# Kernel optimization log

Measured on AMD Instinct MI355X. Metric: run time of the kernel, lower is better.

The kernel has to match this reference:

```python
import jax, jax.numpy as jnp
import numpy as np

B, S, H, F, E, K = 2, 2048, 1024, 4096, 8, 2
NH = H // 128  # heads of dim 128, per SimpleMoEBlock.__init__
DH = H // NH


def _layernorm(x, g, b, eps=1e-5):
    m = x.mean(-1, keepdims=True)
    v = ((x - m) ** 2).mean(-1, keepdims=True)
    return (x - m) / jnp.sqrt(v + eps) * g + b


def _forward(x, ln_attn_g, ln_attn_b, ln_mlp_g, ln_mlp_b,
             in_proj_w, in_proj_b, out_proj_w, out_proj_b,
             router_w, fc1_w, fc1_b, fc2_w, fc2_b):
    # --- self attention (nn.MultiheadAttention, batch_first, no mask) ---
    xa = _layernorm(x, ln_attn_g, ln_attn_b)                    # [B,S,H]
    qkv = xa @ in_proj_w.T + in_proj_b                          # [B,S,3H]
    q, k, v = jnp.split(qkv, 3, axis=-1)
    def heads(t):
        return t.reshape(B, S, NH, DH).transpose(0, 2, 1, 3)    # [B,NH,S,DH]
    q, k, v = heads(q), heads(k), heads(v)
    scores = jnp.einsum('bhqd,bhkd->bhqk', q, k) / jnp.sqrt(jnp.asarray(DH, x.dtype))
    attn = jnp.einsum('bhqk,bhkd->bhqd', jax.nn.softmax(scores, axis=-1), v)
    attn = attn.transpose(0, 2, 1, 3).reshape(B, S, H)
    attn = attn @ out_proj_w.T + out_proj_b
    h = x + attn                                                # residual

    # --- MoE feed-forward ---
    y = _layernorm(h, ln_mlp_g, ln_mlp_b).reshape(B * S, H)     # flat tokens [T,H]
    logits = y @ router_w.T                                     # [T,E]
    probs = jax.nn.softmax(logits, axis=-1)
    top_scores, top_idx = jax.lax.top_k(probs, K)               # [T,K]
    # per-token per-expert combine weight; 0 for unrouted tokens -> identical
    # math to torch's index_select/index_add dispatch
    w = (jax.nn.one_hot(top_idx, E, dtype=y.dtype) * top_scores[..., None]).sum(axis=1)  # [T,E]

    combined = jnp.zeros_like(y)
    for e in range(E):  # fixed small expert count
        he = jax.nn.silu(y @ fc1_w[e].T + fc1_b[e])             # [T,F]
        oe = he @ fc2_w[e].T + fc2_b[e]                         # [T,H]
        combined = combined + oe * w[:, e:e + 1]
    return h + combined.reshape(B, S, H)


def setup_inputs() -> dict:
    key = jax.random.key(0)
    ks = jax.random.split(key, 8)
    s = 0.02
    return {
        'x': jax.random.normal(ks[0], (B, S, H), jnp.float32),
        'ln_attn_g': jnp.ones((H,), jnp.float32),
        'ln_attn_b': jnp.zeros((H,), jnp.float32),
        'ln_mlp_g': jnp.ones((H,), jnp.float32),
        'ln_mlp_b': jnp.zeros((H,), jnp.float32),
        'in_proj_w': jax.random.normal(ks[1], (3 * H, H), jnp.float32) * s,
        'in_proj_b': jnp.zeros((3 * H,), jnp.float32),
        'out_proj_w': jax.random.normal(ks[2], (H, H), jnp.float32) * s,
        'out_proj_b': jnp.zeros((H,), jnp.float32),
        'router_w': jax.random.normal(ks[3], (E, H), jnp.float32) * s,
        'fc1_w': jax.random.normal(ks[4], (E, F, H), jnp.float32) * s,
        'fc1_b': jnp.zeros((E, F), jnp.float32),
        'fc2_w': jax.random.normal(ks[5], (E, H, F), jnp.float32) * s,
        'fc2_b': jnp.zeros((E, H), jnp.float32),
    }


def reference(x, ln_attn_g, ln_attn_b, ln_mlp_g, ln_mlp_b,
              in_proj_w, in_proj_b, out_proj_w, out_proj_b,
              router_w, fc1_w, fc1_b, fc2_w, fc2_b):
    return _forward(x, ln_attn_g, ln_attn_b, ln_mlp_g, ln_mlp_b,
                    in_proj_w, in_proj_b, out_proj_w, out_proj_b,
                    router_w, fc1_w, fc1_b, fc2_w, fc2_b)
```

## Files before the change

### kernel.cpp

```cpp
#include <hip/hip_runtime.h>

#define T_TOK 4096
#define S_SEQ 2048
#define H_DIM 1024
#define H3    3072
#define NHEAD 8
#define DHEAD 128
#define F_DIM 4096
#define NEXP  8
#define MAX_RB 72
#define NSLOT 9216

typedef __bf16 bf16x8 __attribute__((ext_vector_type(8)));
typedef float  f32x4  __attribute__((ext_vector_type(4)));
typedef __attribute__((address_space(1))) const unsigned int* gas1_t;
typedef __attribute__((address_space(3))) unsigned int* las3_t;

__device__ __forceinline__ unsigned short f2bf(float f){
  unsigned int u = __builtin_bit_cast(unsigned int, f);
  u += 0x7fffu + ((u>>16)&1u);
  return (unsigned short)(u>>16);
}
__device__ __forceinline__ float bf2f(unsigned short h){
  unsigned int u = ((unsigned int)h)<<16;
  return __builtin_bit_cast(float, u);
}
__device__ __forceinline__ f32x4 MF(bf16x8 a, bf16x8 b, f32x4 c){
  return __builtin_amdgcn_mfma_f32_16x16x32_bf16(a,b,c,0,0,0);
}
__device__ __forceinline__ void gload16(const void* g, void* l){
  __builtin_amdgcn_global_load_lds((gas1_t)g, (las3_t)l, 16, 0, 0);
}
__device__ __forceinline__ float blockReduceSum(float v){
  __shared__ float sh_red[4];
  #pragma unroll
  for(int o=32;o>0;o>>=1) v += __shfl_down(v,o,64);
  int w = threadIdx.x>>6;
  if((threadIdx.x&63)==0) sh_red[w]=v;
  __syncthreads();
  float tot = sh_red[0]+sh_red[1]+sh_red[2]+sh_red[3];
  __syncthreads();
  return tot;
}

__global__ __launch_bounds__(256) void k_ln_split(const float* __restrict__ x,
    const float* __restrict__ g, const float* __restrict__ bta,
    unsigned short* __restrict__ hi, unsigned short* __restrict__ lo){
  int t = blockIdx.x, tid = threadIdx.x;
  float4 v = reinterpret_cast<const float4*>(x + (size_t)t*H_DIM)[tid];
  float mean = blockReduceSum(v.x+v.y+v.z+v.w) * (1.0f/H_DIM);
  float d0=v.x-mean,d1=v.y-mean,d2=v.z-mean,d3=v.w-mean;
  float var = blockReduceSum(d0*d0+d1*d1+d2*d2+d3*d3) * (1.0f/H_DIM);
  float rstd = rsqrtf(var + 1e-5f);
  float4 gv = reinterpret_cast<const float4*>(g)[tid];
  float4 bv = reinterpret_cast<const float4*>(bta)[tid];
  float o0=d0*rstd*gv.x+bv.x, o1=d1*rstd*gv.y+bv.y, o2=d2*rstd*gv.z+bv.z, o3=d3*rstd*gv.w+bv.w;
  size_t base = (size_t)t*H_DIM + tid*4;
  unsigned short h0=f2bf(o0),h1=f2bf(o1),h2=f2bf(o2),h3=f2bf(o3);
  *reinterpret_cast<ushort4*>(hi+base) = make_ushort4(h0,h1,h2,h3);
  *reinterpret_cast<ushort4*>(lo+base) = make_ushort4(
      f2bf(o0-bf2f(h0)), f2bf(o1-bf2f(h1)), f2bf(o2-bf2f(h2)), f2bf(o3-bf2f(h3)));
}

__global__ __launch_bounds__(256) void k_wsplit(const float* __restrict__ w,
    unsigned short* __restrict__ hi, unsigned short* __restrict__ lo, int n4){
  int i = blockIdx.x*256 + threadIdx.x;
  if(i>=n4) return;
  float4 v = reinterpret_cast<const float4*>(w)[i];
  size_t base = (size_t)i*4;
  unsigned short h0=f2bf(v.x),h1=f2bf(v.y),h2=f2bf(v.z),h3=f2bf(v.w);
  *reinterpret_cast<ushort4*>(hi+base) = make_ushort4(h0,h1,h2,h3);
  *reinterpret_cast<ushort4*>(lo+base) = make_ushort4(
      f2bf(v.x-bf2f(h0)), f2bf(v.y-bf2f(h1)), f2bf(v.z-bf2f(h2)), f2bf(v.w-bf2f(h3)));
}

__global__ __launch_bounds__(256) void k_wconv(const float* __restrict__ w,
    unsigned short* __restrict__ hi, int n4){
  int i = blockIdx.x*256 + threadIdx.x;
  if(i>=n4) return;
  float4 v = reinterpret_cast<const float4*>(w)[i];
  *reinterpret_cast<ushort4*>(hi + (size_t)i*4) =
      make_ushort4(f2bf(v.x), f2bf(v.y), f2bf(v.z), f2bf(v.w));
}

template<int EPI>
__global__ __launch_bounds__(256) void k_gemm_split(
    const unsigned short* __restrict__ Ah, const unsigned short* __restrict__ Al,
    const unsigned short* __restrict__ Bh, const unsigned short* __restrict__ Bl,
    const float* __restrict__ bias, const float* __restrict__ resid,
    unsigned short* __restrict__ Chi, unsigned short* __restrict__ Clo,
    float* __restrict__ Cf, int N, int Kd){
  int m0 = blockIdx.y*128, n0 = blockIdx.x*128;
  int tid=threadIdx.x, wid=tid>>6, lane=tid&63, lr=lane&15, lg=lane>>4;
  int wr=wid>>1, wc=wid&1;
  __shared__ unsigned short tAh[4096], tAl[4096], tBh[4096], tBl[4096];
  f32x4 acc[4][4] = {};
  for(int k0=0;k0<Kd;k0+=32){
    #pragma unroll
    for(int i=0;i<2;i++){
      int p = i*256 + tid;
      int row = p>>2, pc = p&3;
      int lc = pc ^ ((row>>1)&3);
      size_t go = (size_t)row*Kd + k0 + lc*8;
      int lb = (i*256 + wid*64)*8;
      gload16(Ah + (size_t)m0*Kd + go, tAh + lb);
      gload16(Al + (size_t)m0*Kd + go, tAl + lb);
      gload16(Bh + (size_t)n0*Kd + go, tBh + lb);
      gload16(Bl + (size_t)n0*Kd + go, tBl + lb);
    }
    asm volatile("s_waitcnt vmcnt(0)" ::: "memory");
    __syncthreads();
    bf16x8 ah[4], al[4], bh[4], bl[4];
    #pragma unroll
    for(int q=0;q<4;q++){
      int ra = wr*64+q*16+lr;
      int ia = ra*32 + ((lg ^ ((ra>>1)&3))<<3);
      ah[q] = *reinterpret_cast<const bf16x8*>(&tAh[ia]);
      al[q] = *reinterpret_cast<const bf16x8*>(&tAl[ia]);
      int rb = wc*64+q*16+lr;
      int ib = rb*32 + ((lg ^ ((rb>>1)&3))<<3);
      bh[q] = *reinterpret_cast<const bf16x8*>(&tBh[ib]);
      bl[q] = *reinterpret_cast<const bf16x8*>(&tBl[ib]);
    }
    #pragma unroll
    for(int mf=0;mf<4;mf++)
      #pragma unroll
      for(int nf=0;nf<4;nf++){
        acc[mf][nf] = MF(ah[mf], bh[nf], acc[mf][nf]);
        acc[mf][nf] = MF(ah[mf], bl[nf], acc[mf][nf]);
        acc[mf][nf] = MF(al[mf], bh[nf], acc[mf][nf]);
      }
    __syncthreads();
  }
  #pragma unroll
  for(int mf=0;mf<4;mf++)
    #pragma unroll
    for(int nf=0;nf<4;nf++)
      #pragma unroll
      for(int r=0;r<4;r++){
        int row = m0 + wr*64 + mf*16 + lg*4 + r;
        int col = n0 + wc*64 + nf*16 + lr;
        float v = acc[mf][nf][r] + bias[col];
        size_t idx = (size_t)row*N + col;
        if(EPI==0){
          unsigned short hb = f2bf(v);
          Chi[idx]=hb; Clo[idx]=f2bf(v-bf2f(hb));
        } else {
          Cf[idx] = v + resid[idx];
        }
      }
}

__global__ __launch_bounds__(256) void k_vtrans(const unsigned short* __restrict__ qh,
    const unsigned short* __restrict__ ql,
    unsigned short* __restrict__ vth, unsigned short* __restrict__ vtl){
  int bh = blockIdx.z, d0 = blockIdx.y*32, s0 = blockIdx.x*32;
  int b = bh>>3, hh = bh&7;
  int tid=threadIdx.x;
  __shared__ unsigned short th[32][40], tl[32][40];
  int sr = tid>>3, dc = (tid&7)*4;
  size_t src = ((size_t)(b*S_SEQ + s0 + sr))*H3 + 2*H_DIM + hh*DHEAD + d0 + dc;
  *reinterpret_cast<ushort4*>(&th[sr][dc]) = *reinterpret_cast<const ushort4*>(qh+src);
  *reinterpret_cast<ushort4*>(&tl[sr][dc]) = *reinterpret_cast<const ushort4*>(ql+src);
  __syncthreads();
  int dr = tid>>3, sc = (tid&7)*4;
  size_t dst = ((size_t)(bh*DHEAD) + d0+dr)*S_SEQ + s0 + sc;
  *reinterpret_cast<ushort4*>(vth+dst) = make_ushort4(th[sc][dr],th[sc+1][dr],th[sc+2][dr],th[sc+3][dr]);
  *reinterpret_cast<ushort4*>(vtl+dst) = make_ushort4(tl[sc][dr],tl[sc+1][dr],tl[sc+2][dr],tl[sc+3][dr]);
}

__global__ __launch_bounds__(256,1) void k_attn(const unsigned short* __restrict__ qkv_hi,
    const unsigned short* __restrict__ qkv_lo,
    const unsigned short* __restrict__ vt_hi, const unsigned short* __restrict__ vt_lo,
    unsigned short* __restrict__ o_hi, unsigned short* __restrict__ o_lo){
  const float SCALE = 0.08838834764831843f;
  int qb = blockIdx.x, bh = blockIdx.y;
  int b = bh>>3, hh = bh&7;
  int tid=threadIdx.x, wid=tid>>6, lane=tid&63, lr=lane&15, lg=lane>>4;
  __shared__ unsigned short kh[2][4096], kl[2][4096], vh[2][4096], vl[2][4096];
  __shared__ unsigned short ph[4][1024], pl[4][1024];
  int row0 = qb*128 + wid*32;
  bf16x8 qh_[2][4], ql_[2][4];
  #pragma unroll
  for(int j=0;j<2;j++){
    size_t qbase = ((size_t)(b*S_SEQ) + row0 + j*16 + lr)*H3 + hh*DHEAD;
    #pragma unroll
    for(int kk=0;kk<4;kk++){
      qh_[j][kk] = *reinterpret_cast<const bf16x8*>(qkv_hi + qbase + kk*32 + lg*8);
      ql_[j][kk] = *reinterpret_cast<const bf16x8*>(qkv_lo + qbase + kk*32 + lg*8);
    }
  }
  f32x4 o_acc[2][8] = {};
  float mrun[2] = {-1e30f,-1e30f};
  float lrun[2] = {0.f,0.f};

  auto STAGE = [&](int buf, int kv0){
    #pragma unroll
    for(int i=0;i<2;i++){
      int p = i*256 + tid;
      int lb = (i*256 + wid*64)*8;
      {
        int krow = p>>4, pc = p&15;
        int lc = (pc&8)|((pc&7)^(krow&7));
        size_t go = ((size_t)(b*S_SEQ + kv0 + krow))*H3 + H_DIM + hh*DHEAD + lc*8;
        gload16(qkv_hi + go, &kh[buf][lb]);
        gload16(qkv_lo + go, &kl[buf][lb]);
      }
      {
        int vrow = p>>2, pc = p&3;
        int lc = pc ^ ((vrow>>1)&3);
        size_t gv = ((size_t)(bh*DHEAD) + vrow)*S_SEQ + kv0 + lc*8;
        gload16(vt_hi + gv, &vh[buf][lb]);
        gload16(vt_lo + gv, &vl[buf][lb]);
      }
    }
  };

  STAGE(0, 0);
  asm volatile("s_waitcnt vmcnt(0)" ::: "memory");
  __syncthreads();
  int cur = 0;
  for(int kv0=0; kv0<S_SEQ; kv0+=32){
    if(kv0+32 < S_SEQ) STAGE(cur^1, kv0+32);
    f32x4 s0[2] = {}, s1[2] = {};
    #pragma unroll
    for(int kk=0;kk<4;kk++){
      int c = kk*4+lg;
      int phys = (c&8)|((c&7)^(lr&7));
      bf16x8 kah = *reinterpret_cast<const bf16x8*>(&kh[cur][lr*128 + phys*8]);
      bf16x8 kal = *reinterpret_cast<const bf16x8*>(&kl[cur][lr*128 + phys*8]);
      bf16x8 kbh = *reinterpret_cast<const bf16x8*>(&kh[cur][(16+lr)*128 + phys*8]);
      bf16x8 kbl = *reinterpret_cast<const bf16x8*>(&kl[cur][(16+lr)*128 + phys*8]);
      #pragma unroll
      for(int j=0;j<2;j++){
        s0[j] = MF(kah, qh_[j][kk], s0[j]);
        s0[j] = MF(kah, ql_[j][kk], s0[j]);
        s0[j] = MF(kal, qh_[j][kk], s0[j]);
        s1[j] = MF(kbh, qh_[j][kk], s1[j]);
        s1[j] = MF(kbh, ql_[j][kk], s1[j]);
        s1[j] = MF(kbl, qh_[j][kk], s1[j]);
      }
    }
    float sc[2][8]; float mt[2];
    #pragma unroll
    for(int j=0;j<2;j++){
      #pragma unroll
      for(int r=0;r<4;r++){ sc[j][r] = s0[j][r]*SCALE; sc[j][4+r] = s1[j][r]*SCALE; }
      float m_ = fmaxf(fmaxf(fmaxf(sc[j][0],sc[j][1]),fmaxf(sc[j][2],sc[j][3])),
                       fmaxf(fmaxf(sc[j][4],sc[j][5]),fmaxf(sc[j][6],sc[j][7])));
      m_ = fmaxf(m_, __shfl_xor(m_,16,64));
      m_ = fmaxf(m_, __shfl_xor(m_,32,64));
      mt[j] = m_;
    }
    int skip = __all((mt[0] <= mrun[0]+8.0f) && (mt[1] <= mrun[1]+8.0f));
    if(!skip){
      #pragma unroll
      for(int j=0;j<2;j++){
        float mn = fmaxf(mrun[j], mt[j]);
        float rs = __expf(mrun[j]-mn);
        lrun[j] *= rs; mrun[j] = mn;
        #pragma unroll
        for(int nf2=0;nf2<8;nf2++){
          f32x4 t = o_acc[j][nf2];
          t[0]*=rs; t[1]*=rs; t[2]*=rs; t[3]*=rs;
          o_acc[j][nf2] = t;
        }
      }
    }
    #pragma unroll
    for(int j=0;j<2;j++){
      float ssum = 0.f;
      #pragma unroll
      for(int i=0;i<8;i++){ sc[j][i] = __expf(sc[j][i]-mrun[j]); ssum += sc[j][i]; }
      ssum += __shfl_xor(ssum,16,64);
      ssum += __shfl_xor(ssum,32,64);
      lrun[j] += ssum;
      unsigned short hbk[8], lbk[8];
      #pragma unroll
      for(int i=0;i<8;i++){ hbk[i]=f2bf(sc[j][i]); lbk[i]=f2bf(sc[j][i]-bf2f(hbk[i])); }
      int half = (lg&1)*4;
      int a0 = j*512 + lr*32 + (((lg>>1)^(lr&3))<<3) + half;
      int a1 = j*512 + lr*32 + ((((lg>>1)+2)^(lr&3))<<3) + half;
      *reinterpret_cast<ushort4*>(&ph[wid][a0]) = make_ushort4(hbk[0],hbk[1],hbk[2],hbk[3]);
      *reinterpret_cast<ushort4*>(&pl[wid][a0]) = make_ushort4(lbk[0],lbk[1],lbk[2],lbk[3]);
      *reinterpret_cast<ushort4*>(&ph[wid][a1]) = make_ushort4(hbk[4],hbk[5],hbk[6],hbk[7]);
      *reinterpret_cast<ushort4*>(&pl[wid][a1]) = make_ushort4(lbk[4],lbk[5],lbk[6],lbk[7]);
    }
    bf16x8 pbh[2], pbl[2];
    #pragma unroll
    for(int j=0;j<2;j++){
      int pp = (lg^(lr&3))<<3;
      pbh[j] = *reinterpret_cast<const bf16x8*>(&ph[wid][j*512 + lr*32 + pp]);
      pbl[j] = *reinterpret_cast<const bf16x8*>(&pl[wid][j*512 + lr*32 + pp]);
    }
    #pragma unroll
    for(int nf2=0;nf2<8;nf2++){
      int d = nf2*16 + lr;
      int vp = (lg ^ ((lr>>1)&3))<<3;
      bf16x8 vah = *reinterpret_cast<const bf16x8*>(&vh[cur][d*32 + vp]);
      bf16x8 val = *reinterpret_cast<const bf16x8*>(&vl[cur][d*32 + vp]);
      #pragma unroll
      for(int j=0;j<2;j++){
        o_acc[j][nf2] = MF(vah, pbh[j], o_acc[j][nf2]);
        o_acc[j][nf2] = MF(vah, pbl[j], o_acc[j][nf2]);
        o_acc[j][nf2] = MF(val, pbh[j], o_acc[j][nf2]);
      }
    }
    asm volatile("s_waitcnt vmcnt(0)" ::: "memory");
    __syncthreads();
    cur ^= 1;
  }
  #pragma unroll
  for(int j=0;j<2;j++){
    float linv = 1.0f/lrun[j];
    size_t rowg = (size_t)(b*S_SEQ + row0 + j*16 + lr);
    #pragma unroll
    for(int nf2=0;nf2<8;nf2++){
      unsigned short hp[4], lp[4];
      #pragma unroll
      for(int r=0;r<4;r++){
        float v = o_acc[j][nf2][r]*linv;
        hp[r] = f2bf(v); lp[r] = f2bf(v - bf2f(hp[r]));
      }
      size_t idx = rowg*H_DIM + hh*DHEAD + nf2*16 + lg*4;
      *reinterpret_cast<ushort4*>(o_hi+idx) = make_ushort4(hp[0],hp[1],hp[2],hp[3]);
      *reinterpret_cast<ushort4*>(o_lo+idx) = make_ushort4(lp[0],lp[1],lp[2],lp[3]);
    }
  }
}

__global__ __launch_bounds__(256) void k_ln2_router(const float* __restrict__ h,
    const float* __restrict__ g, const float* __restrict__ bt, const float* __restrict__ rw,
    unsigned short* __restrict__ ybf, int* __restrict__ route_e, float* __restrict__ route_w){
  int t = blockIdx.x, tid = threadIdx.x;
  float4 v = reinterpret_cast<const float4*>(h + (size_t)t*H_DIM)[tid];
  float mean = blockReduceSum(v.x+v.y+v.z+v.w) * (1.0f/H_DIM);
  float d0=v.x-mean,d1=v.y-mean,d2=v.z-mean,d3=v.w-mean;
  float var = blockReduceSum(d0*d0+d1*d1+d2*d2+d3*d3) * (1.0f/H_DIM);
  float rstd = rsqrtf(var + 1e-5f);
  float4 gv = reinterpret_cast<const float4*>(g)[tid];
  float4 bv = reinterpret_cast<const float4*>(bt)[tid];
  float o0=d0*rstd*gv.x+bv.x, o1=d1*rstd*gv.y+bv.y, o2=d2*rstd*gv.z+bv.z, o3=d3*rstd*gv.w+bv.w;
  size_t base = (size_t)t*H_DIM + tid*4;
  *reinterpret_cast<ushort4*>(ybf+base) = make_ushort4(f2bf(o0),f2bf(o1),f2bf(o2),f2bf(o3));
  float part[8];
  #pragma unroll
  for(int e=0;e<8;e++){
    float4 r = reinterpret_cast<const float4*>(rw + e*H_DIM)[tid];
    part[e] = o0*r.x + o1*r.y + o2*r.z + o3*r.w;
  }
  __shared__ float sm[32];
  #pragma unroll
  for(int e=0;e<8;e++){
    float p = part[e];
    #pragma unroll
    for(int o=32;o>0;o>>=1) p += __shfl_down(p,o,64);
    if((tid&63)==0) sm[(tid>>6)*8+e] = p;
  }
  __syncthreads();
  if(tid==0){
    float lgt[8];
    #pragma unroll
    for(int e=0;e<8;e++) lgt[e] = sm[e]+sm[8+e]+sm[16+e]+sm[24+e];
    float mx = lgt[0];
    #pragma unroll
    for(int e=1;e<8;e++) mx = fmaxf(mx, lgt[e]);
    float ex[8], ssum=0.f;
    #pragma unroll
    for(int e=0;e<8;e++){ ex[e]=__expf(lgt[e]-mx); ssum+=ex[e]; }
    float inv = 1.0f/ssum;
    int e0=0; float p0=ex[0];
    for(int e=1;e<8;e++) if(ex[e]>p0){p0=ex[e];e0=e;}
    int e1=-1; float p1=-1.0f;
    for(int e=0;e<8;e++) if(e!=e0 && ex[e]>p1){p1=ex[e];e1=e;}
    route_e[2*t]=e0; route_e[2*t+1]=e1;
    route_w[2*t]=p0*inv; route_w[2*t+1]=p1*inv;
  }
}

__global__ __launch_bounds__(256) void k_compact(const int* __restrict__ route_e,
    const float* __restrict__ route_w, int* __restrict__ tok_of_slot,
    float* __restrict__ w_of_slot, int* __restrict__ slot_of_tok,
    int* __restrict__ rb_expert, int* __restrict__ rb_base){
  __shared__ int cnt[8], off[8], pos[8];
  int tid = threadIdx.x;
  if(tid<8){ cnt[tid]=0; pos[tid]=0; }
  __syncthreads();
  for(int t=tid;t<T_TOK;t+=256){
    atomicAdd(&cnt[route_e[2*t]],1);
    atomicAdd(&cnt[route_e[2*t+1]],1);
  }
  __syncthreads();
  if(tid==0){
    int o=0;
    for(int e=0;e<8;e++){ off[e]=o; o += ((cnt[e]+127)>>7)<<7; }
    int rb=0;
    for(int e=0;e<8;e++){
      int nrb = (cnt[e]+127)>>7;
      for(int r=0;r<nrb;r++){ rb_expert[rb]=e; rb_base[rb]=off[e]+r*128; rb++; }
    }
    for(;rb<MAX_RB;rb++){ rb_expert[rb]=-1; rb_base[rb]=0; }
  }
  __syncthreads();
  for(int s=tid;s<NSLOT;s+=256){ tok_of_slot[s]=0; w_of_slot[s]=0.0f; }
  __syncthreads();
  for(int t=tid;t<T_TOK;t+=256){
    int e0=route_e[2*t], e1=route_e[2*t+1];
    int s0 = off[e0] + atomicAdd(&pos[e0],1);
    tok_of_slot[s0]=t; w_of_slot[s0]=route_w[2*t]; slot_of_tok[2*t]=s0;
    int s1 = off[e1] + atomicAdd(&pos[e1],1);
    tok_of_slot[s1]=t; w_of_slot[s1]=route_w[2*t+1]; slot_of_tok[2*t+1]=s1;
  }
}

template<bool FC1, bool PRE>
__global__ __launch_bounds__(256) void k_fc(const unsigned short* __restrict__ Abuf,
    const float* __restrict__ W, const unsigned short* __restrict__ Wbf,
    const float* __restrict__ bias,
    const int* __restrict__ rb_expert, const int* __restrict__ rb_base,
    const int* __restrict__ tok_of_slot, const float* __restrict__ w_of_slot,
    unsigned short* __restrict__ he_out, float* __restrict__ oew_out){
  int rb = blockIdx.y;
  int e = rb_expert[rb];
  if(e<0) return;
  int base = rb_base[rb];
  int n0 = blockIdx.x*128;
  const int Kd = FC1 ? H_DIM : F_DIM;
  const int Nd = FC1 ? F_DIM : H_DIM;
  int tid=threadIdx.x, wid=tid>>6, lane=tid&63, lr=lane&15, lg=lane>>4;
  int wr=wid>>1, wc=wid&1;
  __shared__ unsigned short tA[4096], tB[4096];
  size_t arow_src[2];
  #pragma unroll
  for(int i=0;i<2;i++){
    int row = i*64 + (tid>>2);
    if(FC1){ int tok = tok_of_slot[base+row]; arow_src[i] = (size_t)tok*H_DIM; }
    else   { arow_src[i] = (size_t)(base+row)*F_DIM; }
  }
  const float* Wp = W + (size_t)e*F_DIM*H_DIM;
  const unsigned short* Wbp = Wbf + (size_t)e*F_DIM*H_DIM;
  f32x4 acc[4][4] = {};
  for(int k0=0;k0<Kd;k0+=32){
    #pragma unroll
    for(int i=0;i<2;i++){
      int p = i*256+tid; int row=p>>2, pc=p&3;
      int lc = pc ^ ((row>>1)&3);
      gload16(Abuf + arow_src[i] + k0 + lc*8, tA + (i*256+wid*64)*8);
      if(PRE){
        gload16(Wbp + (size_t)(n0+row)*Kd + k0 + lc*8, tB + (i*256+wid*64)*8);
      }
    }
    if(!PRE){
      #pragma unroll
      for(int j=0;j<4;j++){
        int f = tid*16 + j*4; int row=f>>5; int kin=f&31;
        float4 wv = *reinterpret_cast<const float4*>(Wp + (size_t)(n0+row)*Kd + k0 + kin);
        int c16 = kin>>3, half=(kin>>2)&1;
        int phys = c16 ^ ((row>>1)&3);
        *reinterpret_cast<ushort4*>(&tB[row*32 + phys*8 + half*4]) =
            make_ushort4(f2bf(wv.x), f2bf(wv.y), f2bf(wv.z), f2bf(wv.w));
      }
    }
    asm volatile("s_waitcnt vmcnt(0)" ::: "memory");
    __syncthreads();
    bf16x8 af[4], bfr[4];
    #pragma unroll
    for(int q=0;q<4;q++){
      int ra = wr*64+q*16+lr;
      af[q] = *reinterpret_cast<const bf16x8*>(&tA[ra*32 + ((lg ^ ((ra>>1)&3))<<3)]);
      int rbw = wc*64+q*16+lr;
      bfr[q] = *reinterpret_cast<const bf16x8*>(&tB[rbw*32 + ((lg ^ ((rbw>>1)&3))<<3)]);
    }
    #pragma unroll
    for(int mf=0;mf<4;mf++)
      #pragma unroll
      for(int nf=0;nf<4;nf++)
        acc[mf][nf] = MF(af[mf], bfr[nf], acc[mf][nf]);
    __syncthreads();
  }
  #pragma unroll
  for(int mf=0;mf<4;mf++)
    #pragma unroll
    for(int nf=0;nf<4;nf++)
      #pragma unroll
      for(int r=0;r<4;r++){
        int lrow = wr*64+mf*16+lg*4+r;
        int col = n0 + wc*64+nf*16+lr;
        float v = acc[mf][nf][r] + bias[(size_t)e*Nd + col];
        if(FC1){
          float sv = v/(1.0f+__expf(-v));
          he_out[(size_t)(base+lrow)*F_DIM + col] = f2bf(sv);
        } else {
          oew_out[(size_t)(base+lrow)*H_DIM + col] = w_of_slot[base+lrow]*v;
        }
      }
}

__global__ __launch_bounds__(256) void k_combine(const float* __restrict__ h,
    const float* __restrict__ oew, const int* __restrict__ slot_of_tok,
    float* __restrict__ out){
  int t = blockIdx.x, tid=threadIdx.x;
  int s0 = slot_of_tok[2*t], s1 = slot_of_tok[2*t+1];
  float4 hv = reinterpret_cast<const float4*>(h + (size_t)t*H_DIM)[tid];
  float4 a = reinterpret_cast<const float4*>(oew + (size_t)s0*H_DIM)[tid];
  float4 b = reinterpret_cast<const float4*>(oew + (size_t)s1*H_DIM)[tid];
  float4 o = make_float4(hv.x+a.x+b.x, hv.y+a.y+b.y, hv.z+a.z+b.z, hv.w+a.w+b.w);
  reinterpret_cast<float4*>(out + (size_t)t*H_DIM)[tid] = o;
}

extern "C" void kernel_launch(void* const* d_in, const int* in_sizes, int n_in,
                              void* d_out, int out_size, void* d_ws, size_t ws_size,
                              hipStream_t stream){
  const float* x    = (const float*)d_in[0];
  const float* ln1g = (const float*)d_in[1];
  const float* ln1b = (const float*)d_in[2];
  const float* ln2g = (const float*)d_in[3];
  const float* ln2b = (const float*)d_in[4];
  const float* wqkv = (const float*)d_in[5];
  const float* bqkv = (const float*)d_in[6];
  const float* wout = (const float*)d_in[7];
  const float* bout = (const float*)d_in[8];
  const float* rw   = (const float*)d_in[9];
  const float* fc1w = (const float*)d_in[10];
  const float* fc1b = (const float*)d_in[11];
  const float* fc2w = (const float*)d_in[12];
  const float* fc2b = (const float*)d_in[13];
  char* ws = (char*)d_ws;

  size_t off_ = 0;
  auto AL = [&](size_t bytes){ size_t r = off_; off_ = (off_ + bytes + 255) & ~(size_t)255; return r; };
  size_t o_xa_hi = AL((size_t)T_TOK*H_DIM*2), o_xa_lo = AL((size_t)T_TOK*H_DIM*2);
  size_t o_wq_hi = AL((size_t)H3*H_DIM*2),    o_wq_lo = AL((size_t)H3*H_DIM*2);
  size_t o_wo_hi = AL((size_t)H_DIM*H_DIM*2), o_wo_lo = AL((size_t)H_DIM*H_DIM*2);
  size_t o_qk_hi = AL((size_t)T_TOK*H3*2),    o_qk_lo = AL((size_t)T_TOK*H3*2);
  size_t o_vt_hi = AL((size_t)16*DHEAD*S_SEQ*2), o_vt_lo = AL((size_t)16*DHEAD*S_SEQ*2);
  size_t o_at_hi = AL((size_t)T_TOK*H_DIM*2), o_at_lo = AL((size_t)T_TOK*H_DIM*2);
  size_t o_he  = 0;
  size_t o_oew = (size_t)NSLOT*F_DIM*2;
  size_t o_h   = AL((size_t)T_TOK*H_DIM*4);
  size_t o_ybf = AL((size_t)T_TOK*H_DIM*2);
  size_t o_re  = AL((size_t)T_TOK*2*4);
  size_t o_rwt = AL((size_t)T_TOK*2*4);
  size_t o_st  = AL((size_t)T_TOK*2*4);
  size_t o_ts  = AL((size_t)NSLOT*4);
  size_t o_wsl = AL((size_t)NSLOT*4);
  size_t o_rbe = AL(4096);
  size_t o_rbb = AL(4096);
  size_t o_wb  = AL((size_t)NEXP*F_DIM*H_DIM*2);
  bool pre = (off_ <= ws_size);
  (void)in_sizes; (void)n_in; (void)out_size;

  unsigned short* xa_hi = (unsigned short*)(ws+o_xa_hi);
  unsigned short* xa_lo = (unsigned short*)(ws+o_xa_lo);
  unsigned short* wq_hi = (unsigned short*)(ws+o_wq_hi);
  unsigned short* wq_lo = (unsigned short*)(ws+o_wq_lo);
  unsigned short* wo_hi = (unsigned short*)(ws+o_wo_hi);
  unsigned short* wo_lo = (unsigned short*)(ws+o_wo_lo);
  unsigned short* qk_hi = (unsigned short*)(ws+o_qk_hi);
  unsigned short* qk_lo = (unsigned short*)(ws+o_qk_lo);
  unsigned short* vt_hi = (unsigned short*)(ws+o_vt_hi);
  unsigned short* vt_lo = (unsigned short*)(ws+o_vt_lo);
  unsigned short* at_hi = (unsigned short*)(ws+o_at_hi);
  unsigned short* at_lo = (unsigned short*)(ws+o_at_lo);
  unsigned short* he    = (unsigned short*)(ws+o_he);
  float* oew   = (float*)(ws+o_oew);
  float* hbuf  = (float*)(ws+o_h);
  unsigned short* ybf = (unsigned short*)(ws+o_ybf);
  int*   route_e = (int*)(ws+o_re);
  float* route_w = (float*)(ws+o_rwt);
  int*   slot_of_tok = (int*)(ws+o_st);
  int*   tok_of_slot = (int*)(ws+o_ts);
  float* w_of_slot   = (float*)(ws+o_wsl);
  int*   rb_expert   = (int*)(ws+o_rbe);
  int*   rb_base     = (int*)(ws+o_rbb);
  unsigned short* wb = (unsigned short*)(ws+o_wb);

  k_ln_split<<<T_TOK, 256, 0, stream>>>(x, ln1g, ln1b, xa_hi, xa_lo);
  k_wsplit<<<(H3*H_DIM/4+255)/256, 256, 0, stream>>>(wqkv, wq_hi, wq_lo, H3*H_DIM/4);
  k_wsplit<<<(H_DIM*H_DIM/4+255)/256, 256, 0, stream>>>(wout, wo_hi, wo_lo, H_DIM*H_DIM/4);
  k_gemm_split<0><<<dim3(H3/128, T_TOK/128), 256, 0, stream>>>(
      xa_hi, xa_lo, wq_hi, wq_lo, bqkv, nullptr, qk_hi, qk_lo, nullptr, H3, H_DIM);
  k_vtrans<<<dim3(S_SEQ/32, DHEAD/32, 16), 256, 0, stream>>>(qk_hi, qk_lo, vt_hi, vt_lo);
  k_attn<<<dim3(S_SEQ/128, 16), 256, 0, stream>>>(qk_hi, qk_lo, vt_hi, vt_lo, at_hi, at_lo);
  k_gemm_split<1><<<dim3(H_DIM/128, T_TOK/128), 256, 0, stream>>>(
      at_hi, at_lo, wo_hi, wo_lo, bout, x, nullptr, nullptr, hbuf, H_DIM, H_DIM);
  k_ln2_router<<<T_TOK, 256, 0, stream>>>(hbuf, ln2g, ln2b, rw, ybf, route_e, route_w);
  k_compact<<<1, 256, 0, stream>>>(route_e, route_w, tok_of_slot, w_of_slot,
                                   slot_of_tok, rb_expert, rb_base);
  const int WN4 = NEXP*F_DIM*H_DIM/4;
  if(pre){
    k_wconv<<<(WN4+255)/256, 256, 0, stream>>>(fc1w, wb, WN4);
    k_fc<true,true><<<dim3(F_DIM/128, MAX_RB), 256, 0, stream>>>(
        ybf, fc1w, wb, fc1b, rb_expert, rb_base, tok_of_slot, nullptr, he, nullptr);
    k_wconv<<<(WN4+255)/256, 256, 0, stream>>>(fc2w, wb, WN4);
    k_fc<false,true><<<dim3(H_DIM/128, MAX_RB), 256, 0, stream>>>(
        he, fc2w, wb, fc2b, rb_expert, rb_base, tok_of_slot, w_of_slot, nullptr, oew);
  } else {
    k_fc<true,false><<<dim3(F_DIM/128, MAX_RB), 256, 0, stream>>>(
        ybf, fc1w, wb, fc1b, rb_expert, rb_base, tok_of_slot, nullptr, he, nullptr);
    k_fc<false,false><<<dim3(H_DIM/128, MAX_RB), 256, 0, stream>>>(
        he, fc2w, wb, fc2b, rb_expert, rb_base, tok_of_slot, w_of_slot, nullptr, oew);
  }
  k_combine<<<T_TOK, 256, 0, stream>>>(hbuf, oew, slot_of_tok, (float*)d_out);
}
```

Baseline: 725.4 us.

## Split attention over KV halves with a separate softmax merge kernel

The attention kernel gains a grid z dimension that splits the key/value sequence into chunks. Each chunk writes unnormalized fp32 partial outputs plus running max and sum to a workspace buffer, and a new merge kernel combines them with log-sum-exp rescaling before emitting the hi/lo bf16 split. The original grid had only 256 blocks at one block per CU, which underfills the GPU; splitting doubles the block count. In exchange it adds an extra kernel launch and fp32 partial-result traffic, and it falls back to a single chunk when workspace is short.

```diff
diff --git a/kernel.cpp b/kernel.cpp
--- a/kernel.cpp
+++ b/kernel.cpp
@@ -172,10 +172,11 @@
 __global__ __launch_bounds__(256,1) void k_attn(const unsigned short* __restrict__ qkv_hi,
     const unsigned short* __restrict__ qkv_lo,
     const unsigned short* __restrict__ vt_hi, const unsigned short* __restrict__ vt_lo,
-    unsigned short* __restrict__ o_hi, unsigned short* __restrict__ o_lo){
+    float* __restrict__ opb, float* __restrict__ mlb, int kv_span){
   const float SCALE = 0.08838834764831843f;
-  int qb = blockIdx.x, bh = blockIdx.y;
+  int qb = blockIdx.x, bh = blockIdx.y, zz = blockIdx.z;
   int b = bh>>3, hh = bh&7;
+  int kvbase = zz*kv_span, kvend = kvbase + kv_span;
   int tid=threadIdx.x, wid=tid>>6, lane=tid&63, lr=lane&15, lg=lane>>4;
   __shared__ unsigned short kh[2][4096], kl[2][4096], vh[2][4096], vl[2][4096];
   __shared__ unsigned short ph[4][1024], pl[4][1024];
@@ -216,12 +217,12 @@
     }
   };
 
-  STAGE(0, 0);
+  STAGE(0, kvbase);
   asm volatile("s_waitcnt vmcnt(0)" ::: "memory");
   __syncthreads();
   int cur = 0;
-  for(int kv0=0; kv0<S_SEQ; kv0+=32){
-    if(kv0+32 < S_SEQ) STAGE(cur^1, kv0+32);
+  for(int kv0=kvbase; kv0<kvend; kv0+=32){
+    if(kv0+32 < kvend) STAGE(cur^1, kv0+32);
     f32x4 s0[2] = {}, s1[2] = {};
     #pragma unroll
     for(int kk=0;kk<4;kk++){
@@ -312,21 +313,55 @@
   }
   #pragma unroll
   for(int j=0;j<2;j++){
-    float linv = 1.0f/lrun[j];
-    size_t rowg = (size_t)(b*S_SEQ + row0 + j*16 + lr);
+    int srow = row0 + j*16 + lr;
+    size_t obase = (((size_t)zz*16 + bh)*S_SEQ + srow)*(size_t)DHEAD;
     #pragma unroll
     for(int nf2=0;nf2<8;nf2++){
-      unsigned short hp[4], lp[4];
-      #pragma unroll
-      for(int r=0;r<4;r++){
-        float v = o_acc[j][nf2][r]*linv;
-        hp[r] = f2bf(v); lp[r] = f2bf(v - bf2f(hp[r]));
-      }
-      size_t idx = rowg*H_DIM + hh*DHEAD + nf2*16 + lg*4;
-      *reinterpret_cast<ushort4*>(o_hi+idx) = make_ushort4(hp[0],hp[1],hp[2],hp[3]);
-      *reinterpret_cast<ushort4*>(o_lo+idx) = make_ushort4(lp[0],lp[1],lp[2],lp[3]);
-    }
-  }
+      *reinterpret_cast<f32x4*>(&opb[obase + nf2*16 + lg*4]) = o_acc[j][nf2];
+    }
+    if(lg==0){
+      *reinterpret_cast<float2*>(&mlb[(((size_t)zz*16 + bh)*S_SEQ + srow)*2]) =
+          make_float2(mrun[j], lrun[j]);
+    }
+  }
+}
+
+__global__ __launch_bounds__(256) void k_amerge(const float* __restrict__ opb,
+    const float* __restrict__ mlb, int nz,
+    unsigned short* __restrict__ o_hi, unsigned short* __restrict__ o_lo){
+  int bh = blockIdx.y, b = bh>>3, hh = bh&7;
+  int r = threadIdx.x>>4;
+  int c = (threadIdx.x&15)*8;
+  int srow = blockIdx.x*16 + r;
+  float mz[2], lz[2];
+  float m = -1e30f;
+  for(int z=0;z<nz;z++){
+    const float* mlp = mlb + (((size_t)z*16 + bh)*S_SEQ + srow)*2;
+    mz[z]=mlp[0]; lz[z]=mlp[1];
+    m = fmaxf(m, mz[z]);
+  }
+  float L = 0.f, w[2];
+  for(int z=0;z<nz;z++){ w[z] = __expf(mz[z]-m); L += lz[z]*w[z]; }
+  float linv = 1.0f/L;
+  float acc[8] = {0,0,0,0,0,0,0,0};
+  for(int z=0;z<nz;z++){
+    const float* o = opb + (((size_t)z*16 + bh)*S_SEQ + srow)*(size_t)DHEAD + c;
+    float4 a = *reinterpret_cast<const float4*>(o);
+    float4 bq = *reinterpret_cast<const float4*>(o+4);
+    acc[0]+=a.x*w[z]; acc[1]+=a.y*w[z]; acc[2]+=a.z*w[z]; acc[3]+=a.w*w[z];
+    acc[4]+=bq.x*w[z]; acc[5]+=bq.y*w[z]; acc[6]+=bq.z*w[z]; acc[7]+=bq.w*w[z];
+  }
+  size_t idx = ((size_t)(b*S_SEQ)+srow)*H_DIM + hh*DHEAD + c;
+  unsigned short hp[8], lp[8];
+  #pragma unroll
+  for(int i=0;i<8;i++){
+    float v = acc[i]*linv;
+    hp[i]=f2bf(v); lp[i]=f2bf(v-bf2f(hp[i]));
+  }
+  *reinterpret_cast<ushort4*>(o_hi+idx)   = make_ushort4(hp[0],hp[1],hp[2],hp[3]);
+  *reinterpret_cast<ushort4*>(o_hi+idx+4) = make_ushort4(hp[4],hp[5],hp[6],hp[7]);
+  *reinterpret_cast<ushort4*>(o_lo+idx)   = make_ushort4(lp[0],lp[1],lp[2],lp[3]);
+  *reinterpret_cast<ushort4*>(o_lo+idx+4) = make_ushort4(lp[4],lp[5],lp[6],lp[7]);
 }
 
 __global__ __launch_bounds__(256) void k_ln2_router(const float* __restrict__ h,
@@ -548,6 +583,8 @@
   size_t o_rbb = AL(4096);
   size_t o_wb  = AL((size_t)NEXP*F_DIM*H_DIM*2);
   bool pre = (off_ <= ws_size);
+  size_t o_op  = AL((size_t)2*16*S_SEQ*DHEAD*4 + (size_t)2*16*S_SEQ*2*4 + 256);
+  bool pre2 = (off_ <= ws_size);
   (void)in_sizes; (void)n_in; (void)out_size;
 
   unsigned short* xa_hi = (unsigned short*)(ws+o_xa_hi);
@@ -575,13 +612,19 @@
   int*   rb_base     = (int*)(ws+o_rbb);
   unsigned short* wb = (unsigned short*)(ws+o_wb);
 
+  int nz = pre2 ? 2 : 1;
+  float* opb = pre2 ? (float*)(ws+o_op) : (float*)(ws+o_xa_hi);
+  float* mlb = opb + (size_t)nz*16*S_SEQ*DHEAD;
+
   k_ln_split<<<T_TOK, 256, 0, stream>>>(x, ln1g, ln1b, xa_hi, xa_lo);
   k_wsplit<<<(H3*H_DIM/4+255)/256, 256, 0, stream>>>(wqkv, wq_hi, wq_lo, H3*H_DIM/4);
   k_wsplit<<<(H_DIM*H_DIM/4+255)/256, 256, 0, stream>>>(wout, wo_hi, wo_lo, H_DIM*H_DIM/4);
   k_gemm_split<0><<<dim3(H3/128, T_TOK/128), 256, 0, stream>>>(
       xa_hi, xa_lo, wq_hi, wq_lo, bqkv, nullptr, qk_hi, qk_lo, nullptr, H3, H_DIM);
   k_vtrans<<<dim3(S_SEQ/32, DHEAD/32, 16), 256, 0, stream>>>(qk_hi, qk_lo, vt_hi, vt_lo);
-  k_attn<<<dim3(S_SEQ/128, 16), 256, 0, stream>>>(qk_hi, qk_lo, vt_hi, vt_lo, at_hi, at_lo);
+  k_attn<<<dim3(S_SEQ/128, 16, nz), 256, 0, stream>>>(qk_hi, qk_lo, vt_hi, vt_lo,
+                                                      opb, mlb, S_SEQ/nz);
+  k_amerge<<<dim3(S_SEQ/16, 16), 256, 0, stream>>>(opb, mlb, nz, at_hi, at_lo);
   k_gemm_split<1><<<dim3(H_DIM/128, T_TOK/128), 256, 0, stream>>>(
       at_hi, at_lo, wo_hi, wo_lo, bout, x, nullptr, nullptr, hbuf, H_DIM, H_DIM);
   k_ln2_router<<<T_TOK, 256, 0, stream>>>(hbuf, ln2g, ln2b, rw, ybf, route_e, route_w);
```

Result: no change. 736.2 us (+1.5%).
